# Optimization experiments

Measured on AMD Instinct MI355X. Metric: run time of the kernel, lower is better.

The kernel has to match this reference:

```python
import jax, jax.numpy as jnp
import numpy as np

N_LAYERS = 4
D_MODEL = 1024
EXPAND = 2
D_INNER = EXPAND * D_MODEL
D_STATE = 16
DT_RANK = 64
K_CONV = 4
OUT_DIM = 1024
BATCH = 2
SEQ = 1024
EPS = 1e-5


def setup_inputs() -> dict:
    key = jax.random.key(0)
    ks = jax.random.split(key, 12)
    s = 0.02

    def rn(k, shape, scale=s):
        return jax.random.normal(k, shape, dtype=jnp.float32) * scale

    # Per-layer params stacked along leading n_layers axis (scanned over).
    A_log = jnp.log(jnp.broadcast_to(jnp.arange(1, D_STATE + 1, dtype=jnp.float32),
                                     (N_LAYERS, D_INNER, D_STATE)))
    return {
        "x": jax.random.normal(ks[0], (BATCH, SEQ, D_MODEL), dtype=jnp.float32),
        "norm_w": jnp.ones((N_LAYERS, D_MODEL), jnp.float32),
        "Win": rn(ks[1], (N_LAYERS, D_MODEL, 2 * D_INNER)),
        "conv_w": rn(ks[2], (N_LAYERS, D_INNER, K_CONV), 0.1),
        "conv_b": jnp.zeros((N_LAYERS, D_INNER), jnp.float32),
        "Wx": rn(ks[3], (N_LAYERS, D_INNER, DT_RANK + 2 * D_STATE)),
        "Wdt": rn(ks[4], (N_LAYERS, DT_RANK, D_INNER), 0.1),
        "bdt": rn(ks[5], (N_LAYERS, D_INNER), 0.1),
        "A_log": A_log,
        "Dp": jnp.ones((N_LAYERS, D_INNER), jnp.float32),
        "Wblk": rn(ks[6], (N_LAYERS, D_INNER, D_MODEL)),
        "Wout": rn(ks[7], (D_MODEL, OUT_DIM)),
        "bout": jnp.zeros((OUT_DIM,), jnp.float32),
    }


def _rmsnorm(x, w):
    return x * jax.lax.rsqrt(jnp.mean(x * x, axis=-1, keepdims=True) + EPS) * w


def _causal_depthwise_conv(x, w, b):
    # x: [B, L, D], w: [D, K], b: [D]
    xt = jnp.pad(x, ((0, 0), (K_CONV - 1, 0), (0, 0))).transpose(0, 2, 1)  # [B, D, L+K-1]
    y = jax.lax.conv_general_dilated(
        xt, w[:, None, :], window_strides=(1,), padding='VALID',
        feature_group_count=x.shape[-1], dimension_numbers=('NCH', 'OIH', 'NCH'))
    return y.transpose(0, 2, 1) + b  # [B, L, D]


def _selective_scan(u, delta, A, Bm, Cm, Dp):
    # u, delta: [B, L, Di]; A: [Di, N]; Bm, Cm: [B, L, N]; Dp: [Di]
    def step(h, inp):
        u_t, d_t, b_t, c_t = inp  # [B,Di], [B,Di], [B,N], [B,N]
        dA = jnp.exp(d_t[:, :, None] * A)                    # [B, Di, N]
        h = dA * h + (d_t * u_t)[:, :, None] * b_t[:, None, :]
        y = jnp.einsum('bdn,bn->bd', h, c_t)
        return h, y

    h0 = jnp.zeros((u.shape[0], u.shape[2], A.shape[1]), u.dtype)
    xs = (u.transpose(1, 0, 2), delta.transpose(1, 0, 2),
          Bm.transpose(1, 0, 2), Cm.transpose(1, 0, 2))
    _, ys = jax.lax.scan(step, h0, xs)                        # ys: [L, B, Di]
    return ys.transpose(1, 0, 2) + u * Dp


def _mamba_block(x, p):
    xn = _rmsnorm(x, p['norm_w'])
    xz = xn @ p['Win']                                        # [B, L, 2*Di]
    xp, z = jnp.split(xz, 2, axis=-1)
    xc = jax.nn.silu(_causal_depthwise_conv(xp, p['conv_w'], p['conv_b']))
    dbc = xc @ p['Wx']                                        # [B, L, dt_rank + 2N]
    dt, Bm, Cm = jnp.split(dbc, [DT_RANK, DT_RANK + D_STATE], axis=-1)
    delta = jax.nn.softplus(dt @ p['Wdt'] + p['bdt'])         # [B, L, Di]
    A = -jnp.exp(p['A_log'])                                  # [Di, N]
    y = _selective_scan(xc, delta, A, Bm, Cm, p['Dp'])
    y = y * jax.nn.silu(z)
    return x + y @ p['Wblk']


def reference(x, norm_w, Win, conv_w, conv_b, Wx, Wdt, bdt, A_log, Dp, Wblk, Wout, bout):
    layer_params = {"norm_w": norm_w, "Win": Win, "conv_w": conv_w, "conv_b": conv_b,
                    "Wx": Wx, "Wdt": Wdt, "bdt": bdt, "A_log": A_log,
                    "Dp": Dp, "Wblk": Wblk}

    def layer_step(h, p):
        return _mamba_block(h, p), None

    h, _ = jax.lax.scan(layer_step, x, layer_params)
    return h @ Wout + bout
```

## Files before the change

### kernel.cpp

```cpp
#include <hip/hip_runtime.h>
#include <hip/hip_bf16.h>

#define NLAYERS 4
#define DMODEL 1024
#define DINNER 2048
#define DSTATE 16
#define DTRANK 64
#define KCONV 4
#define OUTDIM 1024
#define BATCH 2
#define SEQ 1024
#define ROWS (BATCH * SEQ)
#define DBC_COLS (DTRANK + 2 * DSTATE)
#define CHUNK 64
#define NCH (SEQ / CHUNK)
#define SPLITK 8
#define KSEG 256

#define DEV __device__ __forceinline__
typedef __hip_bfloat16 bf16;
using bf16x8 = __attribute__((ext_vector_type(8))) short;
using f32x4  = __attribute__((ext_vector_type(4))) float;

DEV float u2f(unsigned short u) { return __uint_as_float(((unsigned)u) << 16); }
DEV unsigned short fb(float f) {
    bf16 h = __float2bfloat16(f);
    return *reinterpret_cast<unsigned short*>(&h);
}
DEV float ld1(const float* p) { return *p; }
DEV float ld1(const bf16* p) { return __bfloat162float(*p); }
DEV float4 ld4(const float* p) { return *reinterpret_cast<const float4*>(p); }
DEV float4 ld4(const bf16* p) {
    ushort4 u = *reinterpret_cast<const ushort4*>(p);
    return make_float4(u2f(u.x), u2f(u.y), u2f(u.z), u2f(u.w));
}
DEV float silu_f(float x) { return x / (1.f + __expf(-x)); }
DEV float softplus_f(float x) { return x > 15.f ? x : log1pf(__expf(x)); }
DEV void store1(float* p, float v) { *p = v; }
DEV void store1(bf16* p, float v) { *p = __float2bfloat16(v); }

__global__ void k_detect(const void* nw, int* flag) {
    if (threadIdx.x == 0 && blockIdx.x == 0) {
        unsigned w = *reinterpret_cast<const unsigned*>(nw);
        *flag = (w == 0x3F803F80u) ? 1 : 0;
    }
}

template <typename WT>
DEV void cast_body(const WT* x, float* h, int n) {
    int i = blockIdx.x * 256 + threadIdx.x;
    if (i < n) h[i] = ld1(x + i);
}
__global__ __launch_bounds__(256) void k_cast(const void* x, float* h, int n, const int* flg) {
    if (*flg) cast_body((const bf16*)x, h, n);
    else      cast_body((const float*)x, h, n);
}

__global__ __launch_bounds__(256) void k_castf2bR(const float* __restrict__ x,
                                                  const float* __restrict__ part,
                                                  bf16* __restrict__ o) {
    int i = blockIdx.x * 256 + threadIdx.x;
    float4 v = reinterpret_cast<const float4*>(x)[i];
    float4 a = reinterpret_cast<const float4*>(part)[i];
    float4 b = reinterpret_cast<const float4*>(part + (size_t)ROWS * DMODEL)[i];
    v.x += a.x + b.x; v.y += a.y + b.y; v.z += a.z + b.z; v.w += a.w + b.w;
    ushort4 u;
    u.x = fb(v.x); u.y = fb(v.y); u.z = fb(v.z); u.w = fb(v.w);
    reinterpret_cast<ushort4*>(o)[i] = u;
}

__global__ __launch_bounds__(256) void k_red(const float* __restrict__ part,
                                             float* __restrict__ dbc,
                                             bf16* __restrict__ dtb) {
    int i = blockIdx.x * 256 + threadIdx.x;
    float s = 0.f;
#pragma unroll
    for (int c = 0; c < SPLITK; c++) s += part[(size_t)c * ROWS * DBC_COLS + i];
    dbc[i] = s;
    int r = i / DBC_COLS, c2 = i - r * DBC_COLS;
    if (c2 < DTRANK) dtb[r * DTRANK + c2] = __float2bfloat16(s);
}

__global__ __launch_bounds__(256) void k_redOut(const float* __restrict__ part,
                                                const void* bias32, const void* bias16,
                                                void* out, const int* flg) {
    int i = blockIdx.x * 256 + threadIdx.x;
    int n = i & (OUTDIM - 1);
    float v = part[i] + part[(size_t)ROWS * OUTDIM + i];
    if (*flg) {
        v += ld1((const bf16*)bias16 + n);
        ((bf16*)out)[i] = __float2bfloat16(v);
    } else {
        v += ld1((const float*)bias32 + n);
        ((float*)out)[i] = v;
    }
}

template <typename WT>
DEV void rms_core(float4 v, const WT* w, int row, int tid, bf16* xn) {
    float ss = v.x * v.x + v.y * v.y + v.z * v.z + v.w * v.w;
#pragma unroll
    for (int off = 1; off < 64; off <<= 1) ss += __shfl_xor(ss, off);
    __shared__ float smem[4];
    if ((tid & 63) == 0) smem[tid >> 6] = ss;
    __syncthreads();
    float tot = smem[0] + smem[1] + smem[2] + smem[3];
    float scale = rsqrtf(tot * (1.f / DMODEL) + 1e-5f);
    float4 wv = ld4(w + tid * 4);
    ushort4 o;
    o.x = fb(v.x * scale * wv.x);
    o.y = fb(v.y * scale * wv.y);
    o.z = fb(v.z * scale * wv.z);
    o.w = fb(v.w * scale * wv.w);
    reinterpret_cast<ushort4*>(xn + (size_t)row * DMODEL)[tid] = o;
}
__global__ __launch_bounds__(256) void k_rmsnorm(const float* h, const void* w32,
                                                 const void* w16, bf16* xn, const int* flg) {
    int row = blockIdx.x, tid = threadIdx.x;
    float4 v = reinterpret_cast<const float4*>(h + (size_t)row * DMODEL)[tid];
    if (*flg) rms_core(v, (const bf16*)w16, row, tid, xn);
    else      rms_core(v, (const float*)w32, row, tid, xn);
}

__global__ __launch_bounds__(256) void k_rmsnormR(float* h, const float* __restrict__ part,
                                                  const void* w32, const void* w16,
                                                  bf16* xn, const int* flg) {
    int row = blockIdx.x, tid = threadIdx.x;
    float* hr = h + (size_t)row * DMODEL;
    const float* pa = part + (size_t)row * DMODEL;
    const float* pb = pa + (size_t)ROWS * DMODEL;
    float4 v = reinterpret_cast<const float4*>(hr)[tid];
    float4 a = reinterpret_cast<const float4*>(pa)[tid];
    float4 b = reinterpret_cast<const float4*>(pb)[tid];
    v.x += a.x + b.x; v.y += a.y + b.y; v.z += a.z + b.z; v.w += a.w + b.w;
    reinterpret_cast<float4*>(hr)[tid] = v;
    if (*flg) rms_core(v, (const bf16*)w16, row, tid, xn);
    else      rms_core(v, (const float*)w32, row, tid, xn);
}

template <typename WT>
DEV void tr_body(const WT* B, bf16* BT, int K, int N, int n0, int k0) {
    __shared__ float tile[32][33];
    int tx = threadIdx.x & 31, ty = threadIdx.x >> 5;
#pragma unroll
    for (int i = 0; i < 4; i++)
        tile[ty + 8 * i][tx] = ld1(&B[(size_t)(k0 + ty + 8 * i) * N + n0 + tx]);
    __syncthreads();
#pragma unroll
    for (int i = 0; i < 4; i++)
        BT[(size_t)(n0 + ty + 8 * i) * K + k0 + tx] = __float2bfloat16(tile[tx][ty + 8 * i]);
}
__global__ __launch_bounds__(256) void k_transpose(const void* B32, const void* B16,
                                                   bf16* BT, int K, int N, const int* flg) {
    int n0 = blockIdx.x * 32, k0 = blockIdx.y * 32;
    if (*flg) tr_body((const bf16*)B16, BT, K, N, n0, k0);
    else      tr_body((const float*)B32, BT, K, N, n0, k0);
}

__global__ __launch_bounds__(256) void k_tr2(const void* Wx32, const void* Wx16,
                                             const void* Wd32, const void* Wd16,
                                             bf16* WxT, bf16* WdT, const int* flg) {
    int bid = blockIdx.x;
    int bfm = *flg;
    if (bid < 128) {
        int n0 = (bid & 63) * 32, k0 = (bid >> 6) * 32;
        if (bfm) tr_body((const bf16*)Wd16, WdT, DTRANK, DINNER, n0, k0);
        else     tr_body((const float*)Wd32, WdT, DTRANK, DINNER, n0, k0);
    } else {
        int r = bid - 128;
        int n0 = (r % 3) * 32, k0 = (r / 3) * 32;
        if (bfm) tr_body((const bf16*)Wx16, WxT, DINNER, DBC_COLS, n0, k0);
        else     tr_body((const float*)Wx32, WxT, DINNER, DBC_COLS, n0, k0);
    }
}

template <bool BIAS, bool NGUARD, bool SOFTPLUS, typename OutT>
__global__ __launch_bounds__(512) void k_mgemm(const bf16* __restrict__ A,
                                               const bf16* __restrict__ BT,
                                               const void* bias32, const void* bias16,
                                               void* Cv, int M, int N, int K, int kseg,
                                               const int* flg) {
    __shared__ __align__(16) bf16 As[2][8192];
    __shared__ __align__(16) bf16 Bs[2][8192];
    int tid = threadIdx.x;
    int wave = tid >> 6, lane = tid & 63;
    int wm = wave >> 1, wn = wave & 1;

    int bx = blockIdx.x, by = blockIdx.y;
    if ((gridDim.x & 7) == 0) {
        int hwid = by * gridDim.x + bx;
        int xcd = hwid & 7;
        int idx = hwid >> 3;
        int sx = gridDim.x >> 3;
        int q = idx / gridDim.y;
        bx = xcd * sx + q;
        by = idx - q * gridDim.y;
    }
    int m0 = by * 128, n0 = bx * 128;
    int bfm = BIAS ? *flg : 0;

    int k_lo = 0;
    int nsteps = K >> 6;
    if (kseg > 0) {
        k_lo = blockIdx.z * kseg;
        nsteps = kseg >> 6;
        Cv = (char*)Cv + (size_t)blockIdx.z * M * N * sizeof(OutT);
    }

    int r8 = lane >> 3, sl = lane & 7;
    int slx = sl ^ r8;
    auto STAGE = [&](int buf, int k0) {
#pragma unroll
        for (int j = 0; j < 2; j++) {
            int R0 = (wave * 2 + j) * 8;
            const bf16* srcA = A + (size_t)(m0 + R0 + r8) * K + k0 + slx * 8;
            const bf16* srcB = BT + (size_t)(n0 + R0 + r8) * K + k0 + slx * 8;
            __builtin_amdgcn_global_load_lds(
                (const __attribute__((address_space(1))) void*)srcA,
                (__attribute__((address_space(3))) void*)((char*)As + buf * 16384 + (wave * 2 + j) * 1024 + lane * 16),
                16, 0, 0);
            __builtin_amdgcn_global_load_lds(
                (const __attribute__((address_space(1))) void*)srcB,
                (__attribute__((address_space(3))) void*)((char*)Bs + buf * 16384 + (wave * 2 + j) * 1024 + lane * 16),
                16, 0, 0);
        }
    };

    f32x4 acc[2][4];
#pragma unroll
    for (int i = 0; i < 2; i++)
#pragma unroll
        for (int j = 0; j < 4; j++) acc[i][j] = {0.f, 0.f, 0.f, 0.f};

    int rl = lane & 15, kcl = lane >> 4;
    int ra = wm * 32 + rl, xa = ra & 7;
    int rb = wn * 64 + rl, xb = rb & 7;

    STAGE(0, k_lo);

    for (int s = 0; s < nsteps; s++) {
        int cur = s & 1;
        asm volatile("s_waitcnt vmcnt(0)" ::: "memory");
        __builtin_amdgcn_s_barrier();
        __builtin_amdgcn_sched_barrier(0);

        if (s + 1 < nsteps) STAGE(cur ^ 1, k_lo + (s + 1) * 64);

        const char* Ab = (const char*)As + cur * 16384;
        const char* Bb = (const char*)Bs + cur * 16384;
        __builtin_amdgcn_s_setprio(1);
#pragma unroll
        for (int c = 0; c < 2; c++) {
            int sa = (((c << 2) + kcl) ^ xa) << 4;
            int sb = (((c << 2) + kcl) ^ xb) << 4;
            bf16x8 af[2], bg[4];
#pragma unroll
            for (int t = 0; t < 2; t++)
                af[t] = *reinterpret_cast<const bf16x8*>(Ab + (ra + t * 16) * 128 + sa);
#pragma unroll
            for (int t = 0; t < 4; t++)
                bg[t] = *reinterpret_cast<const bf16x8*>(Bb + (rb + t * 16) * 128 + sb);
#pragma unroll
            for (int mt = 0; mt < 2; mt++)
#pragma unroll
                for (int nt = 0; nt < 4; nt++)
                    acc[mt][nt] = __builtin_amdgcn_mfma_f32_16x16x32_bf16(
                        af[mt], bg[nt], acc[mt][nt], 0, 0, 0);
        }
        __builtin_amdgcn_s_setprio(0);
    }

    int dcol = lane & 15, dr4 = (lane >> 4) << 2;
#pragma unroll
    for (int mt = 0; mt < 2; mt++) {
#pragma unroll
        for (int nt = 0; nt < 4; nt++) {
            int n = n0 + wn * 64 + nt * 16 + dcol;
            if (NGUARD && n >= N) continue;
#pragma unroll
            for (int r = 0; r < 4; r++) {
                int m = m0 + wm * 32 + mt * 16 + dr4 + r;
                float v = acc[mt][nt][r];
                if (BIAS) v += bfm ? ld1((const bf16*)bias16 + n) : ld1((const float*)bias32 + n);
                if (SOFTPLUS) v = softplus_f(v);
                store1(reinterpret_cast<OutT*>(Cv) + (size_t)m * N + n, v);
            }
        }
    }
}

__global__ __launch_bounds__(256) void k_conv(const bf16* __restrict__ xz,
                                              const void* cw32, const void* cw16,
                                              const void* cb32, const void* cb16,
                                              bf16* __restrict__ xc, const int* flg) {
    int bfm = *flg;
    int i = blockIdx.x * 256 + threadIdx.x;
    int d4 = i & (DINNER / 4 - 1);
    int tg = i >> 9;
    int t0 = (tg & (SEQ / 8 - 1)) * 8;
    int b  = tg >> 7;
    int d  = d4 * 4;

    float wv[4][4];
    if (bfm) {
        const unsigned short* wp = (const unsigned short*)cw16 + d * KCONV;
#pragma unroll
        for (int j = 0; j < 4; j++)
#pragma unroll
            for (int k = 0; k < 4; k++) wv[j][k] = u2f(wp[j * 4 + k]);
    } else {
        const float* wp = (const float*)cw32 + d * KCONV;
#pragma unroll
        for (int j = 0; j < 4; j++)
#pragma unroll
            for (int k = 0; k < 4; k++) wv[j][k] = wp[j * 4 + k];
    }
    float bv[4];
#pragma unroll
    for (int j = 0; j < 4; j++)
        bv[j] = bfm ? ld1((const bf16*)cb16 + d + j) : ld1((const float*)cb32 + d + j);

    const bf16* base = xz + (size_t)(b * SEQ) * (2 * DINNER) + d;
    float xin[11][4];
#pragma unroll
    for (int j = 0; j < 11; j++) {
        int t = t0 - 3 + j;
        if (t >= 0) {
            ushort4 v = *reinterpret_cast<const ushort4*>(base + (size_t)t * (2 * DINNER));
            xin[j][0] = u2f(v.x); xin[j][1] = u2f(v.y);
            xin[j][2] = u2f(v.z); xin[j][3] = u2f(v.w);
        } else {
            xin[j][0] = xin[j][1] = xin[j][2] = xin[j][3] = 0.f;
        }
    }
    bf16* op = xc + (size_t)(b * SEQ + t0) * DINNER + d;
#pragma unroll
    for (int i8 = 0; i8 < 8; i8++) {
        ushort4 o;
        unsigned short* os = reinterpret_cast<unsigned short*>(&o);
#pragma unroll
        for (int j = 0; j < 4; j++) {
            float acc = bv[j];
#pragma unroll
            for (int k = 0; k < 4; k++) acc += xin[i8 + k][j] * wv[j][k];
            os[j] = fb(silu_f(acc));
        }
        *reinterpret_cast<ushort4*>(op + (size_t)i8 * DINNER) = o;
    }
}

__global__ __launch_bounds__(256) void k_scanA(const bf16* __restrict__ u,
                                               const bf16* __restrict__ dlt,
                                               const float* __restrict__ dbc,
                                               const void* Al32, const void* Al16,
                                               const int* flg,
                                               float* __restrict__ Pb,
                                               float* __restrict__ Sb) {
    __shared__ float bc[2][8][32];
    int bid = blockIdx.x;
    int dblk = bid & 7;
    int c = (bid >> 3) & (NCH - 1);
    int b = bid >> 7;
    int tid = threadIdx.x;
    int d = dblk * 256 + tid;
    int bfm = *flg;

    float A[16];
#pragma unroll
    for (int n = 0; n < 16; n++) {
        float al = bfm ? ld1((const bf16*)Al16 + (size_t)d * DSTATE + n)
                       : ld1((const float*)Al32 + (size_t)d * DSTATE + n);
        A[n] = -__expf(al);
    }
    float P[16], S[16];
#pragma unroll
    for (int n = 0; n < 16; n++) { P[n] = 1.f; S[n] = 0.f; }

    const int tbase = c * CHUNK;
    const bf16* up = u + (size_t)(b * SEQ) * DINNER + d;
    const bf16* dp = dlt + (size_t)(b * SEQ) * DINNER + d;

    int srow = tid >> 5, scol = tid & 31;
    bc[0][srow][scol] = dbc[(size_t)(b * SEQ + tbase + srow) * DBC_COLS + DTRANK + scol];
    int cur = 0;
    for (int t8 = 0; t8 < CHUNK; t8 += 8) {
        __syncthreads();
        float dv[8], uv[8];
#pragma unroll
        for (int i = 0; i < 8; i++) {
            int t = tbase + t8 + i;
            dv[i] = ld1(dp + (size_t)t * DINNER);
            uv[i] = ld1(up + (size_t)t * DINNER);
        }
        if (t8 + 8 < CHUNK)
            bc[cur ^ 1][srow][scol] =
                dbc[(size_t)(b * SEQ + tbase + t8 + 8 + srow) * DBC_COLS + DTRANK + scol];
#pragma unroll
        for (int i = 0; i < 8; i++) {
            float bl[16];
            *reinterpret_cast<float4*>(&bl[0])  = *reinterpret_cast<float4*>(&bc[cur][i][0]);
            *reinterpret_cast<float4*>(&bl[4])  = *reinterpret_cast<float4*>(&bc[cur][i][4]);
            *reinterpret_cast<float4*>(&bl[8])  = *reinterpret_cast<float4*>(&bc[cur][i][8]);
            *reinterpret_cast<float4*>(&bl[12]) = *reinterpret_cast<float4*>(&bc[cur][i][12]);
            float x = dv[i] * uv[i];
#pragma unroll
            for (int n = 0; n < 16; n++) {
                float a = __expf(dv[i] * A[n]);
                P[n] *= a;
                S[n] = a * S[n] + x * bl[n];
            }
        }
        cur ^= 1;
    }
    size_t base = ((size_t)(b * NCH + c) * DSTATE) * DINNER + d;
#pragma unroll
    for (int n = 0; n < 16; n++) {
        Pb[base + (size_t)n * DINNER] = P[n];
        Sb[base + (size_t)n * DINNER] = S[n];
    }
}

__global__ __launch_bounds__(256) void k_scanB(const float* __restrict__ Pb,
                                               const float* __restrict__ Sb,
                                               float* __restrict__ Ib) {
    int gid = blockIdx.x * 256 + threadIdx.x;
    int d = gid & (DINNER - 1);
    int n = (gid >> 11) & (DSTATE - 1);
    int b = gid >> 15;
    float H = 0.f;
#pragma unroll
    for (int c = 0; c < NCH; c++) {
        size_t idx = ((size_t)(b * NCH + c) * DSTATE + n) * DINNER + d;
        Ib[idx] = H;
        H = Pb[idx] * H + Sb[idx];
    }
}

__global__ __launch_bounds__(256) void k_scanC(const bf16* __restrict__ u,
                                               bf16* __restrict__ dy,
                                               const float* __restrict__ dbc,
                                               const bf16* __restrict__ xz,
                                               const void* Al32, const void* Al16,
                                               const void* Dp32, const void* Dp16,
                                               const int* flg,
                                               const float* __restrict__ Ib) {
    __shared__ float bc[2][8][32];
    int bid = blockIdx.x;
    int dblk = bid & 7;
    int c = (bid >> 3) & (NCH - 1);
    int b = bid >> 7;
    int tid = threadIdx.x;
    int d = dblk * 256 + tid;
    int bfm = *flg;

    float A[16];
#pragma unroll
    for (int n = 0; n < 16; n++) {
        float al = bfm ? ld1((const bf16*)Al16 + (size_t)d * DSTATE + n)
                       : ld1((const float*)Al32 + (size_t)d * DSTATE + n);
        A[n] = -__expf(al);
    }
    float Dpd = bfm ? ld1((const bf16*)Dp16 + d) : ld1((const float*)Dp32 + d);

    float h[16];
    size_t ibase = ((size_t)(b * NCH + c) * DSTATE) * DINNER + d;
#pragma unroll
    for (int n = 0; n < 16; n++) h[n] = Ib[ibase + (size_t)n * DINNER];

    const int tbase = c * CHUNK;
    const bf16* up = u + (size_t)(b * SEQ) * DINNER + d;
    bf16* dq = dy + (size_t)(b * SEQ) * DINNER + d;
    const bf16* zp = xz + (size_t)(b * SEQ) * (2 * DINNER) + DINNER + d;

    int srow = tid >> 5, scol = tid & 31;
    bc[0][srow][scol] = dbc[(size_t)(b * SEQ + tbase + srow) * DBC_COLS + DTRANK + scol];
    int cur = 0;
    for (int t8 = 0; t8 < CHUNK; t8 += 8) {
        __syncthreads();
        float dv[8], uv[8], zv[8];
#pragma unroll
        for (int i = 0; i < 8; i++) {
            int t = tbase + t8 + i;
            dv[i] = ld1(dq + (size_t)t * DINNER);
            uv[i] = ld1(up + (size_t)t * DINNER);
            zv[i] = ld1(zp + (size_t)t * (2 * DINNER));
        }
        if (t8 + 8 < CHUNK)
            bc[cur ^ 1][srow][scol] =
                dbc[(size_t)(b * SEQ + tbase + t8 + 8 + srow) * DBC_COLS + DTRANK + scol];
#pragma unroll
        for (int i = 0; i < 8; i++) {
            float bl[16], cl[16];
            *reinterpret_cast<float4*>(&bl[0])  = *reinterpret_cast<float4*>(&bc[cur][i][0]);
            *reinterpret_cast<float4*>(&bl[4])  = *reinterpret_cast<float4*>(&bc[cur][i][4]);
            *reinterpret_cast<float4*>(&bl[8])  = *reinterpret_cast<float4*>(&bc[cur][i][8]);
            *reinterpret_cast<float4*>(&bl[12]) = *reinterpret_cast<float4*>(&bc[cur][i][12]);
            *reinterpret_cast<float4*>(&cl[0])  = *reinterpret_cast<float4*>(&bc[cur][i][16]);
            *reinterpret_cast<float4*>(&cl[4])  = *reinterpret_cast<float4*>(&bc[cur][i][20]);
            *reinterpret_cast<float4*>(&cl[8])  = *reinterpret_cast<float4*>(&bc[cur][i][24]);
            *reinterpret_cast<float4*>(&cl[12]) = *reinterpret_cast<float4*>(&bc[cur][i][28]);
            float x = dv[i] * uv[i];
            float s0 = 0.f, s1 = 0.f, s2 = 0.f, s3 = 0.f;
#pragma unroll
            for (int n = 0; n < 16; n++) {
                float a = __expf(dv[i] * A[n]);
                h[n] = a * h[n] + x * bl[n];
                float pp = h[n] * cl[n];
                if ((n & 3) == 0) s0 += pp;
                else if ((n & 3) == 1) s1 += pp;
                else if ((n & 3) == 2) s2 += pp;
                else s3 += pp;
            }
            float s = (s0 + s1) + (s2 + s3);
            float yv = (s + uv[i] * Dpd) * silu_f(zv[i]);
            dq[(size_t)(tbase + t8 + i) * DINNER] = __float2bfloat16(yv);
        }
        cur ^= 1;
    }
}

extern "C" void kernel_launch(void* const* d_in, const int* in_sizes, int n_in,
                              void* d_out, int out_size, void* d_ws, size_t ws_size,
                              hipStream_t stream) {
    const char* x      = (const char*)d_in[0];
    const char* norm_w = (const char*)d_in[1];
    const char* Win    = (const char*)d_in[2];
    const char* conv_w = (const char*)d_in[3];
    const char* conv_b = (const char*)d_in[4];
    const char* Wx     = (const char*)d_in[5];
    const char* Wdt    = (const char*)d_in[6];
    const char* bdt    = (const char*)d_in[7];
    const char* A_log  = (const char*)d_in[8];
    const char* Dp     = (const char*)d_in[9];
    const char* Wblk   = (const char*)d_in[10];
    const char* Wout   = (const char*)d_in[11];
    const char* bout   = (const char*)d_in[12];

    int* flag = (int*)d_ws;
    k_detect<<<1, 64, 0, stream>>>(norm_w, flag);

    const size_t sNw = DMODEL, sWin = (size_t)DMODEL * 2 * DINNER, sCw = (size_t)DINNER * KCONV;
    const size_t sVec = DINNER, sWx = (size_t)DINNER * DBC_COLS, sWdt = (size_t)DTRANK * DINNER;
    const size_t sAl = (size_t)DINNER * DSTATE, sWblk = (size_t)DINNER * DMODEL;

    char* w = (char*)d_ws + 256;
    float* h   = (float*)w; w += (size_t)ROWS * DMODEL * 4;
    float* dbc = (float*)w; w += (size_t)ROWS * DBC_COLS * 4;
    bf16* xn   = (bf16*)w;  w += (size_t)ROWS * DMODEL * 2;
    bf16* xz   = (bf16*)w;  w += (size_t)ROWS * 2 * DINNER * 2;
    bf16* xc   = (bf16*)w;  w += (size_t)ROWS * DINNER * 2;
    bf16* dy   = (bf16*)w;  w += (size_t)ROWS * DINNER * 2;
    bf16* BT   = (bf16*)w;  w += (size_t)4096 * 1024 * 2;
    bf16* dtb  = (bf16*)w;  w += (size_t)ROWS * DTRANK * 2;

    bf16* WdT = (bf16*)((char*)BT + (1 << 19));
    float* partials = (float*)((char*)BT + (1 << 20));
    float* Pb = (float*)BT;
    float* Sb = Pb + (size_t)BATCH * NCH * DSTATE * DINNER;
    float* Ib = (float*)xn;
    float* part2 = (float*)xz;

    const int SCAN_BLKS = BATCH * NCH * (DINNER / 256);

    k_cast<<<(ROWS * DMODEL) / 256, 256, 0, stream>>>(x, h, ROWS * DMODEL, flag);

    for (int l = 0; l < NLAYERS; l++) {
        if (l == 0)
            k_rmsnorm<<<ROWS, 256, 0, stream>>>(
                h, norm_w + l * sNw * 4, norm_w + l * sNw * 2, xn, flag);
        else
            k_rmsnormR<<<ROWS, 256, 0, stream>>>(
                h, part2, norm_w + l * sNw * 4, norm_w + l * sNw * 2, xn, flag);

        k_transpose<<<dim3(4096 / 32, 1024 / 32), 256, 0, stream>>>(
            Win + l * sWin * 4, Win + l * sWin * 2, BT, 1024, 4096, flag);
        k_mgemm<false, false, false, bf16>
            <<<dim3(4096 / 128, ROWS / 128), 512, 0, stream>>>(
            xn, BT, nullptr, nullptr, xz, ROWS, 4096, 1024, 0, flag);

        k_conv<<<(BATCH * (SEQ / 8) * (DINNER / 4)) / 256, 256, 0, stream>>>(
            xz, conv_w + l * sCw * 4, conv_w + l * sCw * 2,
            conv_b + l * sVec * 4, conv_b + l * sVec * 2, xc, flag);

        k_tr2<<<320, 256, 0, stream>>>(
            Wx + l * sWx * 4, Wx + l * sWx * 2,
            Wdt + l * sWdt * 4, Wdt + l * sWdt * 2, BT, WdT, flag);

        k_mgemm<false, true, false, float>
            <<<dim3(1, ROWS / 128, SPLITK), 512, 0, stream>>>(
            xc, BT, nullptr, nullptr, partials, ROWS, DBC_COLS, 2048, KSEG, flag);
        k_red<<<(ROWS * DBC_COLS) / 256, 256, 0, stream>>>(partials, dbc, dtb);

        k_mgemm<true, false, true, bf16>
            <<<dim3(2048 / 128, ROWS / 128), 512, 0, stream>>>(
            dtb, WdT, bdt + l * sVec * 4, bdt + l * sVec * 2,
            dy, ROWS, 2048, DTRANK, 0, flag);

        k_scanA<<<SCAN_BLKS, 256, 0, stream>>>(
            xc, dy, dbc, A_log + l * sAl * 4, A_log + l * sAl * 2, flag, Pb, Sb);
        k_scanB<<<(BATCH * DSTATE * DINNER) / 256, 256, 0, stream>>>(Pb, Sb, Ib);
        k_scanC<<<SCAN_BLKS, 256, 0, stream>>>(
            xc, dy, dbc, xz, A_log + l * sAl * 4, A_log + l * sAl * 2,
            Dp + l * sVec * 4, Dp + l * sVec * 2, flag, Ib);

        k_transpose<<<dim3(1024 / 32, 2048 / 32), 256, 0, stream>>>(
            Wblk + l * sWblk * 4, Wblk + l * sWblk * 2, BT, 2048, 1024, flag);
        k_mgemm<false, false, false, float>
            <<<dim3(1024 / 128, ROWS / 128, 2), 512, 0, stream>>>(
            dy, BT, nullptr, nullptr, part2, ROWS, 1024, 2048, 1024, flag);
    }

    k_castf2bR<<<(ROWS * DMODEL / 4) / 256, 256, 0, stream>>>(h, part2, xn);
    k_transpose<<<dim3(1024 / 32, 1024 / 32), 256, 0, stream>>>(
        Wout, Wout, BT, 1024, 1024, flag);
    k_mgemm<false, false, false, float>
        <<<dim3(1024 / 128, ROWS / 128, 2), 512, 0, stream>>>(
        xn, BT, nullptr, nullptr, part2, ROWS, 1024, 1024, 512, flag);
    k_redOut<<<(ROWS * OUTDIM) / 256, 256, 0, stream>>>(part2, bout, bout, d_out, flag);
}
```

Baseline: 627.4 us.

## Fuse weight transposes into neighboring kernels and split scan state across thread pairs

The per-layer weight transposes now run as extra blocks inside other kernels. The Win transpose joins the RMSNorm kernel, the Wx/Wdt transposes join the conv kernel, and the Wblk transpose joins the scan output kernel. This removes several small launches and their serialization gaps per layer. Separately, the chunked selective-scan kernels now split each channel's 16 states across two threads of 8. That doubles the block count and halves per-thread register state, at the cost of a shuffle reduction and duplicated loads of u, delta and z.

```diff
diff --git a/kernel.cpp b/kernel.cpp
--- a/kernel.cpp
+++ b/kernel.cpp
@@ -114,29 +114,6 @@
     o.w = fb(v.w * scale * wv.w);
     reinterpret_cast<ushort4*>(xn + (size_t)row * DMODEL)[tid] = o;
 }
-__global__ __launch_bounds__(256) void k_rmsnorm(const float* h, const void* w32,
-                                                 const void* w16, bf16* xn, const int* flg) {
-    int row = blockIdx.x, tid = threadIdx.x;
-    float4 v = reinterpret_cast<const float4*>(h + (size_t)row * DMODEL)[tid];
-    if (*flg) rms_core(v, (const bf16*)w16, row, tid, xn);
-    else      rms_core(v, (const float*)w32, row, tid, xn);
-}
-
-__global__ __launch_bounds__(256) void k_rmsnormR(float* h, const float* __restrict__ part,
-                                                  const void* w32, const void* w16,
-                                                  bf16* xn, const int* flg) {
-    int row = blockIdx.x, tid = threadIdx.x;
-    float* hr = h + (size_t)row * DMODEL;
-    const float* pa = part + (size_t)row * DMODEL;
-    const float* pb = pa + (size_t)ROWS * DMODEL;
-    float4 v = reinterpret_cast<const float4*>(hr)[tid];
-    float4 a = reinterpret_cast<const float4*>(pa)[tid];
-    float4 b = reinterpret_cast<const float4*>(pb)[tid];
-    v.x += a.x + b.x; v.y += a.y + b.y; v.z += a.z + b.z; v.w += a.w + b.w;
-    reinterpret_cast<float4*>(hr)[tid] = v;
-    if (*flg) rms_core(v, (const bf16*)w16, row, tid, xn);
-    else      rms_core(v, (const float*)w32, row, tid, xn);
-}
 
 template <typename WT>
 DEV void tr_body(const WT* B, bf16* BT, int K, int N, int n0, int k0) {
@@ -157,20 +134,30 @@
     else      tr_body((const float*)B32, BT, K, N, n0, k0);
 }
 
-__global__ __launch_bounds__(256) void k_tr2(const void* Wx32, const void* Wx16,
-                                             const void* Wd32, const void* Wd16,
-                                             bf16* WxT, bf16* WdT, const int* flg) {
-    int bid = blockIdx.x;
+template <bool ADD>
+__global__ __launch_bounds__(256) void k_pre(float* h, const float* __restrict__ part,
+                                             const void* w32, const void* w16, bf16* xn,
+                                             const void* Wi32, const void* Wi16, bf16* WinT,
+                                             const int* flg) {
+    int bid = blockIdx.x, tid = threadIdx.x;
     int bfm = *flg;
-    if (bid < 128) {
-        int n0 = (bid & 63) * 32, k0 = (bid >> 6) * 32;
-        if (bfm) tr_body((const bf16*)Wd16, WdT, DTRANK, DINNER, n0, k0);
-        else     tr_body((const float*)Wd32, WdT, DTRANK, DINNER, n0, k0);
+    if (bid < ROWS) {
+        float* hr = h + (size_t)bid * DMODEL;
+        float4 v = reinterpret_cast<const float4*>(hr)[tid];
+        if (ADD) {
+            const float* pa = part + (size_t)bid * DMODEL;
+            float4 a = reinterpret_cast<const float4*>(pa)[tid];
+            float4 b = reinterpret_cast<const float4*>(pa + (size_t)ROWS * DMODEL)[tid];
+            v.x += a.x + b.x; v.y += a.y + b.y; v.z += a.z + b.z; v.w += a.w + b.w;
+            reinterpret_cast<float4*>(hr)[tid] = v;
+        }
+        if (bfm) rms_core(v, (const bf16*)w16, bid, tid, xn);
+        else     rms_core(v, (const float*)w32, bid, tid, xn);
     } else {
-        int r = bid - 128;
-        int n0 = (r % 3) * 32, k0 = (r / 3) * 32;
-        if (bfm) tr_body((const bf16*)Wx16, WxT, DINNER, DBC_COLS, n0, k0);
-        else     tr_body((const float*)Wx32, WxT, DINNER, DBC_COLS, n0, k0);
+        int r = bid - ROWS;
+        int n0 = (r & 127) * 32, k0 = (r >> 7) * 32;
+        if (bfm) tr_body((const bf16*)Wi16, WinT, DMODEL, 2 * DINNER, n0, k0);
+        else     tr_body((const float*)Wi32, WinT, DMODEL, 2 * DINNER, n0, k0);
     }
 }
 
@@ -289,12 +276,9 @@
     }
 }
 
-__global__ __launch_bounds__(256) void k_conv(const bf16* __restrict__ xz,
-                                              const void* cw32, const void* cw16,
-                                              const void* cb32, const void* cb16,
-                                              bf16* __restrict__ xc, const int* flg) {
-    int bfm = *flg;
-    int i = blockIdx.x * 256 + threadIdx.x;
+DEV void conv_body(int i, int bfm, const bf16* __restrict__ xz,
+                   const void* cw32, const void* cw16,
+                   const void* cb32, const void* cb16, bf16* __restrict__ xc) {
     int d4 = i & (DINNER / 4 - 1);
     int tg = i >> 9;
     int t0 = (tg & (SEQ / 8 - 1)) * 8;
@@ -348,6 +332,31 @@
         *reinterpret_cast<ushort4*>(op + (size_t)i8 * DINNER) = o;
     }
 }
+
+__global__ __launch_bounds__(256) void k_convtr(const bf16* __restrict__ xz,
+                                                const void* cw32, const void* cw16,
+                                                const void* cb32, const void* cb16,
+                                                bf16* __restrict__ xc,
+                                                const void* Wx32, const void* Wx16,
+                                                const void* Wd32, const void* Wd16,
+                                                bf16* WxT, bf16* WdT, const int* flg) {
+    int bid = blockIdx.x;
+    int bfm = *flg;
+    if (bid < 512) {
+        conv_body(bid * 256 + threadIdx.x, bfm, xz, cw32, cw16, cb32, cb16, xc);
+    } else if (bid < 640) {
+        int r = bid - 512;
+        int n0 = (r & 63) * 32, k0 = (r >> 6) * 32;
+        if (bfm) tr_body((const bf16*)Wd16, WdT, DTRANK, DINNER, n0, k0);
+        else     tr_body((const float*)Wd32, WdT, DTRANK, DINNER, n0, k0);
+    } else {
+        int r = bid - 640;
+        int n0 = (r % 3) * 32, k0 = (r / 3) * 32;
+        if (bfm) tr_body((const bf16*)Wx16, WxT, DINNER, DBC_COLS, n0, k0);
+        else     tr_body((const float*)Wx32, WxT, DINNER, DBC_COLS, n0, k0);
+    }
+}
+
 
 __global__ __launch_bounds__(256) void k_scanA(const bf16* __restrict__ u,
                                                const bf16* __restrict__ dlt,
@@ -358,23 +367,25 @@
                                                float* __restrict__ Sb) {
     __shared__ float bc[2][8][32];
     int bid = blockIdx.x;
-    int dblk = bid & 7;
-    int c = (bid >> 3) & (NCH - 1);
-    int b = bid >> 7;
+    int dblk = bid & 15;
+    int c = (bid >> 4) & (NCH - 1);
+    int b = bid >> 8;
     int tid = threadIdx.x;
-    int d = dblk * 256 + tid;
+    int nh = tid & 1, dl = tid >> 1;
+    int d = dblk * 128 + dl;
+    int n0 = nh * 8;
     int bfm = *flg;
 
-    float A[16];
-#pragma unroll
-    for (int n = 0; n < 16; n++) {
-        float al = bfm ? ld1((const bf16*)Al16 + (size_t)d * DSTATE + n)
-                       : ld1((const float*)Al32 + (size_t)d * DSTATE + n);
-        A[n] = -__expf(al);
-    }
-    float P[16], S[16];
-#pragma unroll
-    for (int n = 0; n < 16; n++) { P[n] = 1.f; S[n] = 0.f; }
+    float A[8];
+#pragma unroll
+    for (int j = 0; j < 8; j++) {
+        float al = bfm ? ld1((const bf16*)Al16 + (size_t)d * DSTATE + n0 + j)
+                       : ld1((const float*)Al32 + (size_t)d * DSTATE + n0 + j);
+        A[j] = -__expf(al);
+    }
+    float P[8], S[8];
+#pragma unroll
+    for (int j = 0; j < 8; j++) { P[j] = 1.f; S[j] = 0.f; }
 
     const int tbase = c * CHUNK;
     const bf16* up = u + (size_t)(b * SEQ) * DINNER + d;
@@ -397,26 +408,24 @@
                 dbc[(size_t)(b * SEQ + tbase + t8 + 8 + srow) * DBC_COLS + DTRANK + scol];
 #pragma unroll
         for (int i = 0; i < 8; i++) {
-            float bl[16];
-            *reinterpret_cast<float4*>(&bl[0])  = *reinterpret_cast<float4*>(&bc[cur][i][0]);
-            *reinterpret_cast<float4*>(&bl[4])  = *reinterpret_cast<float4*>(&bc[cur][i][4]);
-            *reinterpret_cast<float4*>(&bl[8])  = *reinterpret_cast<float4*>(&bc[cur][i][8]);
-            *reinterpret_cast<float4*>(&bl[12]) = *reinterpret_cast<float4*>(&bc[cur][i][12]);
+            float bl[8];
+            *reinterpret_cast<float4*>(&bl[0]) = *reinterpret_cast<float4*>(&bc[cur][i][n0]);
+            *reinterpret_cast<float4*>(&bl[4]) = *reinterpret_cast<float4*>(&bc[cur][i][n0 + 4]);
             float x = dv[i] * uv[i];
 #pragma unroll
-            for (int n = 0; n < 16; n++) {
-                float a = __expf(dv[i] * A[n]);
-                P[n] *= a;
-                S[n] = a * S[n] + x * bl[n];
+            for (int j = 0; j < 8; j++) {
+                float a = __expf(dv[i] * A[j]);
+                P[j] *= a;
+                S[j] = a * S[j] + x * bl[j];
             }
         }
         cur ^= 1;
     }
     size_t base = ((size_t)(b * NCH + c) * DSTATE) * DINNER + d;
 #pragma unroll
-    for (int n = 0; n < 16; n++) {
-        Pb[base + (size_t)n * DINNER] = P[n];
-        Sb[base + (size_t)n * DINNER] = S[n];
+    for (int j = 0; j < 8; j++) {
+        Pb[base + (size_t)(n0 + j) * DINNER] = P[j];
+        Sb[base + (size_t)(n0 + j) * DINNER] = S[j];
     }
 }
 
@@ -436,36 +445,47 @@
     }
 }
 
-__global__ __launch_bounds__(256) void k_scanC(const bf16* __restrict__ u,
-                                               bf16* __restrict__ dy,
-                                               const float* __restrict__ dbc,
-                                               const bf16* __restrict__ xz,
-                                               const void* Al32, const void* Al16,
-                                               const void* Dp32, const void* Dp16,
-                                               const int* flg,
-                                               const float* __restrict__ Ib) {
+__global__ __launch_bounds__(256) void k_scanCW(const bf16* __restrict__ u,
+                                                bf16* __restrict__ dy,
+                                                const float* __restrict__ dbc,
+                                                const bf16* __restrict__ xz,
+                                                const void* Al32, const void* Al16,
+                                                const void* Dp32, const void* Dp16,
+                                                const int* flg,
+                                                const float* __restrict__ Ib,
+                                                const void* Wb32, const void* Wb16,
+                                                bf16* WbT) {
     __shared__ float bc[2][8][32];
     int bid = blockIdx.x;
-    int dblk = bid & 7;
-    int c = (bid >> 3) & (NCH - 1);
-    int b = bid >> 7;
+    int bfm = *flg;
+    if (bid >= 512) {
+        int r = bid - 512;
+        int n0 = (r & 31) * 32, k0 = (r >> 5) * 32;
+        if (bfm) tr_body((const bf16*)Wb16, WbT, DINNER, DMODEL, n0, k0);
+        else     tr_body((const float*)Wb32, WbT, DINNER, DMODEL, n0, k0);
+        return;
+    }
+    int dblk = bid & 15;
+    int c = (bid >> 4) & (NCH - 1);
+    int b = bid >> 8;
     int tid = threadIdx.x;
-    int d = dblk * 256 + tid;
-    int bfm = *flg;
-
-    float A[16];
-#pragma unroll
-    for (int n = 0; n < 16; n++) {
-        float al = bfm ? ld1((const bf16*)Al16 + (size_t)d * DSTATE + n)
-                       : ld1((const float*)Al32 + (size_t)d * DSTATE + n);
-        A[n] = -__expf(al);
+    int nh = tid & 1, dl = tid >> 1;
+    int d = dblk * 128 + dl;
+    int n0 = nh * 8;
+
+    float A[8];
+#pragma unroll
+    for (int j = 0; j < 8; j++) {
+        float al = bfm ? ld1((const bf16*)Al16 + (size_t)d * DSTATE + n0 + j)
+                       : ld1((const float*)Al32 + (size_t)d * DSTATE + n0 + j);
+        A[j] = -__expf(al);
     }
     float Dpd = bfm ? ld1((const bf16*)Dp16 + d) : ld1((const float*)Dp32 + d);
 
-    float h[16];
+    float h[8];
     size_t ibase = ((size_t)(b * NCH + c) * DSTATE) * DINNER + d;
 #pragma unroll
-    for (int n = 0; n < 16; n++) h[n] = Ib[ibase + (size_t)n * DINNER];
+    for (int j = 0; j < 8; j++) h[j] = Ib[ibase + (size_t)(n0 + j) * DINNER];
 
     const int tbase = c * CHUNK;
     const bf16* up = u + (size_t)(b * SEQ) * DINNER + d;
@@ -490,30 +510,27 @@
                 dbc[(size_t)(b * SEQ + tbase + t8 + 8 + srow) * DBC_COLS + DTRANK + scol];
 #pragma unroll
         for (int i = 0; i < 8; i++) {
-            float bl[16], cl[16];
-            *reinterpret_cast<float4*>(&bl[0])  = *reinterpret_cast<float4*>(&bc[cur][i][0]);
-            *reinterpret_cast<float4*>(&bl[4])  = *reinterpret_cast<float4*>(&bc[cur][i][4]);
-            *reinterpret_cast<float4*>(&bl[8])  = *reinterpret_cast<float4*>(&bc[cur][i][8]);
-            *reinterpret_cast<float4*>(&bl[12]) = *reinterpret_cast<float4*>(&bc[cur][i][12]);
-            *reinterpret_cast<float4*>(&cl[0])  = *reinterpret_cast<float4*>(&bc[cur][i][16]);
-            *reinterpret_cast<float4*>(&cl[4])  = *reinterpret_cast<float4*>(&bc[cur][i][20]);
-            *reinterpret_cast<float4*>(&cl[8])  = *reinterpret_cast<float4*>(&bc[cur][i][24]);
-            *reinterpret_cast<float4*>(&cl[12]) = *reinterpret_cast<float4*>(&bc[cur][i][28]);
+            float bl[8], cl[8];
+            *reinterpret_cast<float4*>(&bl[0]) = *reinterpret_cast<float4*>(&bc[cur][i][n0]);
+            *reinterpret_cast<float4*>(&bl[4]) = *reinterpret_cast<float4*>(&bc[cur][i][n0 + 4]);
+            *reinterpret_cast<float4*>(&cl[0]) = *reinterpret_cast<float4*>(&bc[cur][i][16 + n0]);
+            *reinterpret_cast<float4*>(&cl[4]) = *reinterpret_cast<float4*>(&bc[cur][i][16 + n0 + 4]);
             float x = dv[i] * uv[i];
             float s0 = 0.f, s1 = 0.f, s2 = 0.f, s3 = 0.f;
 #pragma unroll
-            for (int n = 0; n < 16; n++) {
-                float a = __expf(dv[i] * A[n]);
-                h[n] = a * h[n] + x * bl[n];
-                float pp = h[n] * cl[n];
-                if ((n & 3) == 0) s0 += pp;
-                else if ((n & 3) == 1) s1 += pp;
-                else if ((n & 3) == 2) s2 += pp;
+            for (int j = 0; j < 8; j++) {
+                float a = __expf(dv[i] * A[j]);
+                h[j] = a * h[j] + x * bl[j];
+                float pp = h[j] * cl[j];
+                if ((j & 3) == 0) s0 += pp;
+                else if ((j & 3) == 1) s1 += pp;
+                else if ((j & 3) == 2) s2 += pp;
                 else s3 += pp;
             }
-            float s = (s0 + s1) + (s2 + s3);
+            float sh = (s0 + s1) + (s2 + s3);
+            float s = sh + __shfl_xor(sh, 1);
             float yv = (s + uv[i] * Dpd) * silu_f(zv[i]);
-            dq[(size_t)(tbase + t8 + i) * DINNER] = __float2bfloat16(yv);
+            if (nh == 0) dq[(size_t)(tbase + t8 + i) * DINNER] = __float2bfloat16(yv);
         }
         cur ^= 1;
     }
@@ -560,29 +577,25 @@
     float* Ib = (float*)xn;
     float* part2 = (float*)xz;
 
-    const int SCAN_BLKS = BATCH * NCH * (DINNER / 256);
-
     k_cast<<<(ROWS * DMODEL) / 256, 256, 0, stream>>>(x, h, ROWS * DMODEL, flag);
 
     for (int l = 0; l < NLAYERS; l++) {
         if (l == 0)
-            k_rmsnorm<<<ROWS, 256, 0, stream>>>(
-                h, norm_w + l * sNw * 4, norm_w + l * sNw * 2, xn, flag);
+            k_pre<false><<<ROWS + 4096, 256, 0, stream>>>(
+                h, part2, norm_w + l * sNw * 4, norm_w + l * sNw * 2, xn,
+                Win + l * sWin * 4, Win + l * sWin * 2, BT, flag);
         else
-            k_rmsnormR<<<ROWS, 256, 0, stream>>>(
-                h, part2, norm_w + l * sNw * 4, norm_w + l * sNw * 2, xn, flag);
-
-        k_transpose<<<dim3(4096 / 32, 1024 / 32), 256, 0, stream>>>(
-            Win + l * sWin * 4, Win + l * sWin * 2, BT, 1024, 4096, flag);
+            k_pre<true><<<ROWS + 4096, 256, 0, stream>>>(
+                h, part2, norm_w + l * sNw * 4, norm_w + l * sNw * 2, xn,
+                Win + l * sWin * 4, Win + l * sWin * 2, BT, flag);
+
         k_mgemm<false, false, false, bf16>
             <<<dim3(4096 / 128, ROWS / 128), 512, 0, stream>>>(
             xn, BT, nullptr, nullptr, xz, ROWS, 4096, 1024, 0, flag);
 
-        k_conv<<<(BATCH * (SEQ / 8) * (DINNER / 4)) / 256, 256, 0, stream>>>(
+        k_convtr<<<832, 256, 0, stream>>>(
             xz, conv_w + l * sCw * 4, conv_w + l * sCw * 2,
-            conv_b + l * sVec * 4, conv_b + l * sVec * 2, xc, flag);
-
-        k_tr2<<<320, 256, 0, stream>>>(
+            conv_b + l * sVec * 4, conv_b + l * sVec * 2, xc,
             Wx + l * sWx * 4, Wx + l * sWx * 2,
             Wdt + l * sWdt * 4, Wdt + l * sWdt * 2, BT, WdT, flag);
 
@@ -596,15 +609,14 @@
             dtb, WdT, bdt + l * sVec * 4, bdt + l * sVec * 2,
             dy, ROWS, 2048, DTRANK, 0, flag);
 
-        k_scanA<<<SCAN_BLKS, 256, 0, stream>>>(
+        k_scanA<<<512, 256, 0, stream>>>(
             xc, dy, dbc, A_log + l * sAl * 4, A_log + l * sAl * 2, flag, Pb, Sb);
         k_scanB<<<(BATCH * DSTATE * DINNER) / 256, 256, 0, stream>>>(Pb, Sb, Ib);
-        k_scanC<<<SCAN_BLKS, 256, 0, stream>>>(
+        k_scanCW<<<2560, 256, 0, stream>>>(
             xc, dy, dbc, xz, A_log + l * sAl * 4, A_log + l * sAl * 2,
-            Dp + l * sVec * 4, Dp + l * sVec * 2, flag, Ib);
-
-        k_transpose<<<dim3(1024 / 32, 2048 / 32), 256, 0, stream>>>(
-            Wblk + l * sWblk * 4, Wblk + l * sWblk * 2, BT, 2048, 1024, flag);
+            Dp + l * sVec * 4, Dp + l * sVec * 2, flag, Ib,
+            Wblk + l * sWblk * 4, Wblk + l * sWblk * 2, BT);
+
         k_mgemm<false, false, false, float>
             <<<dim3(1024 / 128, ROWS / 128, 2), 512, 0, stream>>>(
             dy, BT, nullptr, nullptr, part2, ROWS, 1024, 2048, 1024, flag);
```

Measured after the change: 599.7 us. 1.05x faster.
